# Kernel optimization log

Measured on AMD Instinct MI355X. Metric: run time of the kernel, lower is better.

The kernel has to match this reference:

```python
import jax, jax.numpy as jnp
import numpy as np

N_BITS = 8
LEVELS = 2 ** N_BITS - 1  # 255 quantization levels (asymmetric uniform)
EPS = 1e-8


def _round_ste(x):
    # straight-through round (forward: round, backward: identity)
    return x + jax.lax.stop_gradient(jnp.round(x) - x)


def _fake_quant_uniform(x):
    # dynamic per-tensor asymmetric uniform quantization (UniformQuantizer)
    xmin = jnp.min(x)
    xmax = jnp.max(x)
    scale = jnp.maximum((xmax - xmin) / LEVELS, EPS)
    zero_point = jnp.round(-xmin / scale)
    x_int = jnp.clip(_round_ste(x / scale) + zero_point, 0, LEVELS)
    return (x_int - zero_point) * scale


def setup_inputs() -> dict:
    key = jax.random.key(0)
    kA, kB = jax.random.split(key)
    A = jax.random.normal(kA, (4, 4096, 4096), dtype=jnp.float32)  # [batch, M, K]
    B = jax.random.normal(kB, (4096, 4096), dtype=jnp.float32)     # [K, N]
    return {"A": A, "B": B}


def reference(A, B):
    # QuantMatMul.forward with use_input_quant=True, use_weight_quant=True
    Aq = _fake_quant_uniform(A)
    Bq = _fake_quant_uniform(B)
    return Aq @ Bq  # [batch, M, N]
```

## Files before the change

kernel.cpp:

```cpp
#include <hip/hip_runtime.h>


#define K_DIM 4096
#define N_COLS 4096
#define M_ROWS 16384

typedef __attribute__((ext_vector_type(4))) int int4v;
typedef __attribute__((ext_vector_type(16))) int int16v;

static const size_t OFF_AQ = 0;
static const size_t OFF_BT = (size_t)64 << 20;
static const size_t OFF_RS = OFF_BT + ((size_t)16 << 20);
static const size_t OFF_CS = OFF_RS + (size_t)M_ROWS * 4;
static const size_t OFF_MM = OFF_CS + (size_t)N_COLS * 4;

__device__ __forceinline__ unsigned enc_f(float f) {
  unsigned u = __float_as_uint(f);
  return (u & 0x80000000u) ? ~u : (u | 0x80000000u);
}
__device__ __forceinline__ float dec_f(unsigned e) {
  unsigned u = (e & 0x80000000u) ? (e & 0x7fffffffu) : ~e;
  return __uint_as_float(u);
}

__device__ __forceinline__ int quantize1(float x, float r, float zp) {
  return (int)(fminf(fmaxf(rintf(x * r) + zp, 0.0f), 255.0f)) - 128;
}

__device__ __forceinline__ void gload16(const void* g, void* l) {
  __builtin_amdgcn_global_load_lds(
      (const __attribute__((address_space(1))) unsigned int*)g,
      (__attribute__((address_space(3))) unsigned int*)l, 16, 0, 0);
}

__device__ __forceinline__ void qparams_a(const unsigned* mm, float& ra, float& zpa) {
  const float amin = dec_f(mm[0]), amax = dec_f(mm[1]);
  const float sa = fmaxf((amax - amin) / 255.0f, 1e-8f);
  zpa = rintf(-amin / sa);
  ra = 1.0f / sa;
}
__device__ __forceinline__ void qparams_b(const unsigned* mm, float& rb, float& zpb) {
  const float bmin = dec_f(mm[2]), bmax = dec_f(mm[3]);
  const float sb = fmaxf((bmax - bmin) / 255.0f, 1e-8f);
  zpb = rintf(-bmin / sb);
  rb = 1.0f / sb;
}

__global__ __launch_bounds__(256) void init_k(unsigned* __restrict__ mm,
                                              int* __restrict__ colsum) {
  const int i = blockIdx.x * 256 + threadIdx.x;
  if (i < N_COLS) colsum[i] = 0;
  if (i == N_COLS) {
    mm[0] = 0xFFFFFFFFu; mm[1] = 0u;
    mm[2] = 0xFFFFFFFFu; mm[3] = 0u;
  }
}

__global__ __launch_bounds__(256) void minmax_k(const float4* __restrict__ A,
                                                const float4* __restrict__ B,
                                                unsigned* __restrict__ mm) {
  const bool isB = blockIdx.x >= 4096;
  const float4* __restrict__ x = isB ? B : A;
  const int bid = isB ? (int)blockIdx.x - 4096 : (int)blockIdx.x;
  unsigned* m = mm + (isB ? 2 : 0);
  const int t = threadIdx.x;
  const long i0 = (long)bid * 256 + t;
  const long STR = isB ? (long)1024 * 256 : (long)4096 * 256;

  float lo = 3.402823466e38f, hi = -3.402823466e38f;
#pragma unroll
  for (int g = 0; g < 4; ++g) {
    float4 v0 = x[i0 + (long)(4 * g + 0) * STR];
    float4 v1 = x[i0 + (long)(4 * g + 1) * STR];
    float4 v2 = x[i0 + (long)(4 * g + 2) * STR];
    float4 v3 = x[i0 + (long)(4 * g + 3) * STR];
    lo = fminf(lo, fminf(fminf(v0.x, v0.y), fminf(v0.z, v0.w)));
    hi = fmaxf(hi, fmaxf(fmaxf(v0.x, v0.y), fmaxf(v0.z, v0.w)));
    lo = fminf(lo, fminf(fminf(v1.x, v1.y), fminf(v1.z, v1.w)));
    hi = fmaxf(hi, fmaxf(fmaxf(v1.x, v1.y), fmaxf(v1.z, v1.w)));
    lo = fminf(lo, fminf(fminf(v2.x, v2.y), fminf(v2.z, v2.w)));
    hi = fmaxf(hi, fmaxf(fmaxf(v2.x, v2.y), fmaxf(v2.z, v2.w)));
    lo = fminf(lo, fminf(fminf(v3.x, v3.y), fminf(v3.z, v3.w)));
    hi = fmaxf(hi, fmaxf(fmaxf(v3.x, v3.y), fmaxf(v3.z, v3.w)));
  }
  for (int off = 32; off; off >>= 1) {
    lo = fminf(lo, __shfl_down(lo, off));
    hi = fmaxf(hi, __shfl_down(hi, off));
  }
  __shared__ float slo[4], shi[4];
  if ((t & 63) == 0) { slo[t >> 6] = lo; shi[t >> 6] = hi; }
  __syncthreads();
  if (t == 0) {
    for (int w = 1; w < 4; w++) { lo = fminf(lo, slo[w]); hi = fmaxf(hi, shi[w]); }
    atomicMin(&m[0], enc_f(lo));
    atomicMax(&m[1], enc_f(hi));
  }
}

__global__ __launch_bounds__(256) void prep2_k(const float* __restrict__ A,
                                               const float* __restrict__ B,
                                               signed char* __restrict__ Aq,
                                               signed char* __restrict__ Bt,
                                               int* __restrict__ rowsum,
                                               int* __restrict__ colsum,
                                               const unsigned* __restrict__ mm) {
  __shared__ unsigned char s[64][72];
  __shared__ int sw[4];
  const int t = threadIdx.x;
  const int bid = blockIdx.x;

  if (bid < 2048) {
    float ra, zpa;
    qparams_a(mm, ra, zpa);
#pragma unroll 1
    for (int rr = 0; rr < 8; ++rr) {
      const int row = bid * 8 + rr;
      const float4* src = (const float4*)(A + (size_t)row * K_DIM);
      unsigned* dst = (unsigned*)(Aq + (size_t)row * K_DIM);
      int sum = 0;
#pragma unroll
      for (int j = 0; j < 4; j++) {
        const int d = j * 256 + t;
        float4 v = src[d];
        int q0 = quantize1(v.x, ra, zpa);
        int q1 = quantize1(v.y, ra, zpa);
        int q2 = quantize1(v.z, ra, zpa);
        int q3 = quantize1(v.w, ra, zpa);
        sum += q0 + q1 + q2 + q3;
        dst[d] = ((unsigned)q0 & 255u) | (((unsigned)q1 & 255u) << 8) |
                 (((unsigned)q2 & 255u) << 16) | (((unsigned)q3 & 255u) << 24);
      }
      for (int off = 32; off; off >>= 1) sum += __shfl_down(sum, off);
      if ((t & 63) == 0) sw[t >> 6] = sum;
      __syncthreads();
      if (t == 0) rowsum[row] = sw[0] + sw[1] + sw[2] + sw[3];
      __syncthreads();
    }
  } else {
    float rb, zpb;
    qparams_b(mm, rb, zpb);
    const int kr = t >> 2, tl = t & 3;
    const int nr = t >> 2, kb = tl * 16;
#pragma unroll 1
    for (int j8 = 0; j8 < 8; ++j8) {
      const int ti = (bid - 2048) * 8 + j8;
      const int n0 = (ti & 63) * 64, k0 = (ti >> 6) * 64;
      const float* rowp = B + (size_t)(k0 + kr) * N_COLS + n0;
#pragma unroll
      for (int j = 0; j < 4; j++) {
        const int fi = tl + j * 4;
        float4 v = *(const float4*)(rowp + fi * 4);
        int q0 = quantize1(v.x, rb, zpb);
        int q1 = quantize1(v.y, rb, zpb);
        int q2 = quantize1(v.z, rb, zpb);
        int q3 = quantize1(v.w, rb, zpb);
        *(unsigned*)&s[kr][fi * 4] = ((unsigned)q0 & 255u) | (((unsigned)q1 & 255u) << 8) |
                                     (((unsigned)q2 & 255u) << 16) | (((unsigned)q3 & 255u) << 24);
      }
      __syncthreads();
      unsigned w[4];
      int psum = 0;
#pragma unroll
      for (int jj = 0; jj < 4; jj++) {
        unsigned b0 = s[kb + jj * 4 + 0][nr];
        unsigned b1 = s[kb + jj * 4 + 1][nr];
        unsigned b2 = s[kb + jj * 4 + 2][nr];
        unsigned b3 = s[kb + jj * 4 + 3][nr];
        w[jj] = b0 | (b1 << 8) | (b2 << 16) | (b3 << 24);
        psum += (int)(signed char)b0 + (int)(signed char)b1 +
                (int)(signed char)b2 + (int)(signed char)b3;
      }
      int4v o = {(int)w[0], (int)w[1], (int)w[2], (int)w[3]};
      *(int4v*)(Bt + (size_t)(n0 + nr) * K_DIM + (k0 + kb)) = o;
      psum += __shfl_xor(psum, 1);
      psum += __shfl_xor(psum, 2);
      if (tl == 0) atomicAdd(&colsum[n0 + nr], psum);
      __syncthreads();
    }
  }
}

__global__ __launch_bounds__(512, 2) void gemm_k(const signed char* __restrict__ Aq,
                                                 const signed char* __restrict__ Bt,
                                                 float* __restrict__ C,
                                                 const int* __restrict__ rowsum,
                                                 const int* __restrict__ colsum,
                                                 const unsigned* __restrict__ mm) {
  __shared__ signed char lds[131072];
  const int t = threadIdx.x;

  const int orig = blockIdx.x;
  const int wgid = (orig & 7) * 128 + (orig >> 3);
  const int m0 = (wgid >> 4) * 256;
  const int n0 = (wgid & 15) * 256;

  const int w = t >> 6, l = t & 63;
  const int wm4 = (w >> 2) * 32;
  const int wn4 = (w & 3) * 16;
  const int r32 = l & 31, h = l >> 5;
  const int u = r32 >> 2, c4 = (r32 & 3) * 4;

  unsigned aAddr[4][2], bAddr[2][2];
#pragma unroll
  for (int mi = 0; mi < 4; ++mi)
#pragma unroll
    for (int kk = 0; kk < 2; ++kk)
      aAddr[mi][kk] = (unsigned)(wm4 + 8 * mi + u) * 256 +
                      ((unsigned)((c4 + 2 * kk + h) ^ u) << 4);
#pragma unroll
  for (int ni = 0; ni < 2; ++ni)
#pragma unroll
    for (int kk = 0; kk < 2; ++kk)
      bAddr[ni][kk] = 16384u + (unsigned)(wn4 + 8 * ni + u) * 256 +
                      ((unsigned)((c4 + 2 * kk + h) ^ u) << 4);

  const int bs_ = t & 15, Rq = t >> 4;
  const int b16 = bs_ ^ (Rq & 7);
  const int sc = b16 >> 2, slb = b16 & 3;
  const signed char* pA0 = Aq + (size_t)(m0 + 4 * Rq + sc) * K_DIM + slb * 16;
  const signed char* pA1 = pA0 + (size_t)128 * K_DIM;
  const signed char* pB0 = Bt + (size_t)(n0 + 4 * Rq + sc) * K_DIM + slb * 16;
  const signed char* pB1 = pB0 + (size_t)128 * K_DIM;

  int16v acc[4][2] = {};

#define STAGE_A(SN) do {                                  \
    gload16(pA0, lds + (SN) + t * 16);                    \
    gload16(pA1, lds + (SN) + 8192 + t * 16);             \
    pA0 += 64; pA1 += 64; } while (0)
#define STAGE_B(SN) do {                                  \
    gload16(pB0, lds + (SN) + 16384 + t * 16);            \
    gload16(pB1, lds + (SN) + 24576 + t * 16);            \
    pB0 += 64; pB1 += 64; } while (0)

#define MM_(A, B, CC) CC = __builtin_amdgcn_mfma_i32_32x32x32_i8(A, B, CC, 0, 0, 0)

#define RD6(SC, KK)                                                  \
    int4v b0 = *(const int4v*)(lds + (SC) + bAddr[0][KK]);           \
    int4v b1 = *(const int4v*)(lds + (SC) + bAddr[1][KK]);           \
    int4v a0 = *(const int4v*)(lds + (SC) + aAddr[0][KK]);           \
    int4v a1 = *(const int4v*)(lds + (SC) + aAddr[1][KK]);           \
    int4v a2 = *(const int4v*)(lds + (SC) + aAddr[2][KK]);           \
    int4v a3 = *(const int4v*)(lds + (SC) + aAddr[3][KK]);

#define MFMA8                                                        \
    __builtin_amdgcn_s_setprio(1);                                   \
    MM_(a0, b0, acc[0][0]); MM_(a0, b1, acc[0][1]);                  \
    MM_(a1, b0, acc[1][0]); MM_(a1, b1, acc[1][1]);                  \
    MM_(a2, b0, acc[2][0]); MM_(a2, b1, acc[2][1]);                  \
    MM_(a3, b0, acc[3][0]); MM_(a3, b1, acc[3][1]);                  \
    __builtin_amdgcn_s_setprio(0);

#define WAITN(N) asm volatile("s_waitcnt vmcnt(" #N ")" ::: "memory")
#define SBAR do { __builtin_amdgcn_sched_barrier(0);                 \
                  __builtin_amdgcn_s_barrier();                      \
                  __builtin_amdgcn_sched_barrier(0); } while (0)

#define HALF(SC, SN, ENDW) do {                                      \
    { RD6(SC, 0) STAGE_A(SN); SBAR; MFMA8 } SBAR;                    \
    { RD6(SC, 1) STAGE_B(SN); SBAR; MFMA8 } ENDW; SBAR;              \
  } while (0)
#define HALF_NS(SC, ENDW) do {                                       \
    { RD6(SC, 0) SBAR; MFMA8 } SBAR;                                 \
    { RD6(SC, 1) SBAR; MFMA8 } ENDW; SBAR;                           \
  } while (0)

  STAGE_A(0);     STAGE_B(0);
  STAGE_A(32768); STAGE_B(32768);
  STAGE_A(65536); STAGE_B(65536);
  WAITN(8); SBAR;

#pragma unroll 1
  for (int g = 0; g < 15; ++g) {
    HALF(0,     98304, WAITN(8));
    HALF(32768, 0,     WAITN(8));
    HALF(65536, 32768, WAITN(8));
    HALF(98304, 65536, WAITN(8));
  }
  HALF(0, 98304, WAITN(8));
  HALF_NS(32768, WAITN(4));
  HALF_NS(65536, WAITN(0));
  HALF_NS(98304, );

#undef STAGE_A
#undef STAGE_B
#undef MM_
#undef RD6
#undef MFMA8
#undef WAITN
#undef SBAR
#undef HALF
#undef HALF_NS

  const float amin = dec_f(mm[0]), amax = dec_f(mm[1]);
  const float bmin = dec_f(mm[2]), bmax = dec_f(mm[3]);
  const float sa = fmaxf((amax - amin) / 255.0f, 1e-8f);
  const float sb = fmaxf((bmax - bmin) / 255.0f, 1e-8f);
  const int za = (int)rintf(-amin / sa) - 128;
  const int zb = (int)rintf(-bmin / sb) - 128;
  const float sab = sa * sb;
  const int kzz = K_DIM * za * zb;
  const int wm = wm4 * 4, wn = wn4 * 4;
  const int col0 = n0 + wn + r32;
  const int cs0 = za * colsum[col0];
  const int cs1 = za * colsum[col0 + 32];
#pragma unroll
  for (int mi = 0; mi < 4; ++mi) {
    const int rbase = m0 + wm + mi * 32 + 4 * h;
#pragma unroll
    for (int r = 0; r < 16; ++r) {
      const int row = rbase + (r & 3) + 8 * (r >> 2);
      const int base = kzz - zb * rowsum[row];
      C[(size_t)row * N_COLS + col0]      = sab * (float)(acc[mi][0][r] + base - cs0);
      C[(size_t)row * N_COLS + col0 + 32] = sab * (float)(acc[mi][1][r] + base - cs1);
    }
  }
}

extern "C" void kernel_launch(void* const* d_in, const int* in_sizes, int n_in,
                              void* d_out, int out_size, void* d_ws, size_t ws_size,
                              hipStream_t stream) {
  const float* A = (const float*)d_in[0];
  const float* B = (const float*)d_in[1];
  float* C = (float*)d_out;
  char* ws = (char*)d_ws;
  signed char* Aq = (signed char*)(ws + OFF_AQ);
  signed char* Bt = (signed char*)(ws + OFF_BT);
  int* rowsum = (int*)(ws + OFF_RS);
  int* colsum = (int*)(ws + OFF_CS);
  unsigned* mm = (unsigned*)(ws + OFF_MM);

  init_k<<<17, 256, 0, stream>>>(mm, colsum);
  minmax_k<<<5120, 256, 0, stream>>>((const float4*)A, (const float4*)B, mm);
  prep2_k<<<2560, 256, 0, stream>>>(A, B, Aq, Bt, rowsum, colsum, mm);
  gemm_k<<<1024, 512, 0, stream>>>(Aq, Bt, C, rowsum, colsum, mm);
}
```

Before: 835.1 us.

## Load B fragments directly from global into registers, halve LDS staging

B tiles are no longer staged through shared memory. Each wave loads its own B MFMA fragments straight from global memory into registers with inline global_load_dwordx4, double-buffered across the two k-halves. Only A goes through LDS, so the LDS buffer is halved to 64KB, which removes B LDS reads and writes and may allow more occupancy. The trade is that each B element is now fetched by every wave sharing that column (uncoalesced-ish, more L2 traffic), and the hand-written vmcnt wait counts make the code fragile.

Result: slower. 988.4 us (+18.4%).

```diff
diff --git a/kernel.cpp b/kernel.cpp
--- a/kernel.cpp
+++ b/kernel.cpp
@@ -186,7 +186,7 @@
                                                  const int* __restrict__ rowsum,
                                                  const int* __restrict__ colsum,
                                                  const unsigned* __restrict__ mm) {
-  __shared__ signed char lds[131072];
+  __shared__ signed char lds[65536];
   const int t = threadIdx.x;
 
   const int orig = blockIdx.x;
@@ -196,22 +196,16 @@
 
   const int w = t >> 6, l = t & 63;
   const int wm4 = (w >> 2) * 32;
-  const int wn4 = (w & 3) * 16;
+  const int wn = (w & 3) * 64;
   const int r32 = l & 31, h = l >> 5;
   const int u = r32 >> 2, c4 = (r32 & 3) * 4;
 
-  unsigned aAddr[4][2], bAddr[2][2];
+  unsigned aAddr[4][2];
 #pragma unroll
   for (int mi = 0; mi < 4; ++mi)
 #pragma unroll
     for (int kk = 0; kk < 2; ++kk)
       aAddr[mi][kk] = (unsigned)(wm4 + 8 * mi + u) * 256 +
-                      ((unsigned)((c4 + 2 * kk + h) ^ u) << 4);
-#pragma unroll
-  for (int ni = 0; ni < 2; ++ni)
-#pragma unroll
-    for (int kk = 0; kk < 2; ++kk)
-      bAddr[ni][kk] = 16384u + (unsigned)(wn4 + 8 * ni + u) * 256 +
                       ((unsigned)((c4 + 2 * kk + h) ^ u) << 4);
 
   const int bs_ = t & 15, Rq = t >> 4;
@@ -219,78 +213,108 @@
   const int sc = b16 >> 2, slb = b16 & 3;
   const signed char* pA0 = Aq + (size_t)(m0 + 4 * Rq + sc) * K_DIM + slb * 16;
   const signed char* pA1 = pA0 + (size_t)128 * K_DIM;
-  const signed char* pB0 = Bt + (size_t)(n0 + 4 * Rq + sc) * K_DIM + slb * 16;
-  const signed char* pB1 = pB0 + (size_t)128 * K_DIM;
+
+  const signed char* pBf0 = Bt + (size_t)(n0 + wn + r32) * K_DIM + h * 16;
+  const signed char* pBf1 = pBf0 + (size_t)32 * K_DIM;
 
   int16v acc[4][2] = {};
+  int4v a0, a1, a2, a3;
+  int4v b0, b1, b2, b3;
 
 #define STAGE_A(SN) do {                                  \
     gload16(pA0, lds + (SN) + t * 16);                    \
     gload16(pA1, lds + (SN) + 8192 + t * 16);             \
     pA0 += 64; pA1 += 64; } while (0)
-#define STAGE_B(SN) do {                                  \
-    gload16(pB0, lds + (SN) + 16384 + t * 16);            \
-    gload16(pB1, lds + (SN) + 24576 + t * 16);            \
-    pB0 += 64; pB1 += 64; } while (0)
+
+#define LOADB(DST, PTR, OFF)                                         \
+    asm volatile("global_load_dwordx4 %0, %1, off offset:" #OFF      \
+                 : "=v"(DST) : "v"(PTR))
 
 #define MM_(A, B, CC) CC = __builtin_amdgcn_mfma_i32_32x32x32_i8(A, B, CC, 0, 0, 0)
 
-#define RD6(SC, KK)                                                  \
-    int4v b0 = *(const int4v*)(lds + (SC) + bAddr[0][KK]);           \
-    int4v b1 = *(const int4v*)(lds + (SC) + bAddr[1][KK]);           \
-    int4v a0 = *(const int4v*)(lds + (SC) + aAddr[0][KK]);           \
-    int4v a1 = *(const int4v*)(lds + (SC) + aAddr[1][KK]);           \
-    int4v a2 = *(const int4v*)(lds + (SC) + aAddr[2][KK]);           \
-    int4v a3 = *(const int4v*)(lds + (SC) + aAddr[3][KK]);
-
-#define MFMA8                                                        \
+#define RDA(SC, KK)                                                  \
+    a0 = *(const int4v*)(lds + (SC) + aAddr[0][KK]);                 \
+    a1 = *(const int4v*)(lds + (SC) + aAddr[1][KK]);                 \
+    a2 = *(const int4v*)(lds + (SC) + aAddr[2][KK]);                 \
+    a3 = *(const int4v*)(lds + (SC) + aAddr[3][KK]);
+
+#define MFMA8(B0, B1)                                                \
     __builtin_amdgcn_s_setprio(1);                                   \
-    MM_(a0, b0, acc[0][0]); MM_(a0, b1, acc[0][1]);                  \
-    MM_(a1, b0, acc[1][0]); MM_(a1, b1, acc[1][1]);                  \
-    MM_(a2, b0, acc[2][0]); MM_(a2, b1, acc[2][1]);                  \
-    MM_(a3, b0, acc[3][0]); MM_(a3, b1, acc[3][1]);                  \
+    MM_(a0, B0, acc[0][0]); MM_(a0, B1, acc[0][1]);                  \
+    MM_(a1, B0, acc[1][0]); MM_(a1, B1, acc[1][1]);                  \
+    MM_(a2, B0, acc[2][0]); MM_(a2, B1, acc[2][1]);                  \
+    MM_(a3, B0, acc[3][0]); MM_(a3, B1, acc[3][1]);                  \
     __builtin_amdgcn_s_setprio(0);
 
 #define WAITN(N) asm volatile("s_waitcnt vmcnt(" #N ")" ::: "memory")
-#define SBAR do { __builtin_amdgcn_sched_barrier(0);                 \
-                  __builtin_amdgcn_s_barrier();                      \
-                  __builtin_amdgcn_sched_barrier(0); } while (0)
-
-#define HALF(SC, SN, ENDW) do {                                      \
-    { RD6(SC, 0) STAGE_A(SN); SBAR; MFMA8 } SBAR;                    \
-    { RD6(SC, 1) STAGE_B(SN); SBAR; MFMA8 } ENDW; SBAR;              \
+#define SCHED0 __builtin_amdgcn_sched_barrier(0)
+#define SBAR do { SCHED0; __builtin_amdgcn_s_barrier(); SCHED0; } while (0)
+
+#define HALF_F(SC, SN) do {                                          \
+    WAITN(4); SBAR;                                                  \
+    RDA(SC, 0)                                                       \
+    MFMA8(b0, b1)                                                    \
+    LOADB(b0, pBf0, 0); LOADB(b1, pBf1, 0);                          \
+    RDA(SC, 1)                                                       \
+    WAITN(4); SCHED0;                                                \
+    MFMA8(b2, b3)                                                    \
+    LOADB(b2, pBf0, 32); LOADB(b3, pBf1, 32);                        \
+    pBf0 += 64; pBf1 += 64;                                          \
+    SCHED0; STAGE_A(SN);                                             \
+    SBAR;                                                            \
   } while (0)
-#define HALF_NS(SC, ENDW) do {                                       \
-    { RD6(SC, 0) SBAR; MFMA8 } SBAR;                                 \
-    { RD6(SC, 1) SBAR; MFMA8 } ENDW; SBAR;                           \
+#define HALF_B(SC, W1N, W2N) do {                                    \
+    WAITN(W1N); SBAR;                                                \
+    RDA(SC, 0)                                                       \
+    MFMA8(b0, b1)                                                    \
+    LOADB(b0, pBf0, 0); LOADB(b1, pBf1, 0);                          \
+    RDA(SC, 1)                                                       \
+    WAITN(W2N); SCHED0;                                              \
+    MFMA8(b2, b3)                                                    \
+    LOADB(b2, pBf0, 32); LOADB(b3, pBf1, 32);                        \
+    pBf0 += 64; pBf1 += 64;                                          \
+    SBAR;                                                            \
   } while (0)
-
-  STAGE_A(0);     STAGE_B(0);
-  STAGE_A(32768); STAGE_B(32768);
-  STAGE_A(65536); STAGE_B(65536);
-  WAITN(8); SBAR;
+#define HALF_L(SC) do {                                              \
+    WAITN(2); SBAR;                                                  \
+    RDA(SC, 0)                                                       \
+    MFMA8(b0, b1)                                                    \
+    RDA(SC, 1)                                                       \
+    WAITN(0); SCHED0;                                                \
+    MFMA8(b2, b3)                                                    \
+  } while (0)
+
+  STAGE_A(0); STAGE_A(16384);
+  SCHED0;
+  LOADB(b0, pBf0, 0);  LOADB(b1, pBf1, 0);
+  LOADB(b2, pBf0, 32); LOADB(b3, pBf1, 32);
+  pBf0 += 64; pBf1 += 64;
+  SCHED0;
+  STAGE_A(32768);
 
 #pragma unroll 1
   for (int g = 0; g < 15; ++g) {
-    HALF(0,     98304, WAITN(8));
-    HALF(32768, 0,     WAITN(8));
-    HALF(65536, 32768, WAITN(8));
-    HALF(98304, 65536, WAITN(8));
-  }
-  HALF(0, 98304, WAITN(8));
-  HALF_NS(32768, WAITN(4));
-  HALF_NS(65536, WAITN(0));
-  HALF_NS(98304, );
+    HALF_F(0, 49152);
+    HALF_F(16384, 0);
+    HALF_F(32768, 16384);
+    HALF_F(49152, 32768);
+  }
+  HALF_F(0, 49152);
+  HALF_B(16384, 4, 4);
+  HALF_B(32768, 2, 2);
+  HALF_L(49152);
 
 #undef STAGE_A
-#undef STAGE_B
+#undef LOADB
 #undef MM_
-#undef RD6
+#undef RDA
 #undef MFMA8
 #undef WAITN
+#undef SCHED0
 #undef SBAR
-#undef HALF
-#undef HALF_NS
+#undef HALF_F
+#undef HALF_B
+#undef HALF_L
 
   const float amin = dec_f(mm[0]), amax = dec_f(mm[1]);
   const float bmin = dec_f(mm[2]), bmax = dec_f(mm[3]);
@@ -300,7 +324,7 @@
   const int zb = (int)rintf(-bmin / sb) - 128;
   const float sab = sa * sb;
   const int kzz = K_DIM * za * zb;
-  const int wm = wm4 * 4, wn = wn4 * 4;
+  const int wm = wm4 * 4;
   const int col0 = n0 + wn + r32;
   const int cs0 = za * colsum[col0];
   const int cs1 = za * colsum[col0 + 32];
```
